# Kernel optimization log

Measured on AMD Instinct MI355X. Metric: run time of the kernel, lower is better.

## Reference

```python
import jax, jax.numpy as jnp
import numpy as np
import math

N_HEAD = 4
NORM_GROUPS = 32
EPS = 1e-5


def setup_inputs() -> dict:
    key = jax.random.key(0)
    ks = jax.random.split(key, 6)
    C = 256
    x = jax.random.normal(ks[0], (2, C, 64, 64), dtype=jnp.float32)
    gn_w = jnp.ones((C,), dtype=jnp.float32)
    gn_b = jnp.zeros((C,), dtype=jnp.float32)
    s = 1.0 / math.sqrt(C)
    wq = jax.random.normal(ks[1], (C, C), dtype=jnp.float32) * s
    wk = jax.random.normal(ks[2], (C, C), dtype=jnp.float32) * s
    wv = jax.random.normal(ks[3], (C, C), dtype=jnp.float32) * s
    wo = jax.random.normal(ks[4], (C, C), dtype=jnp.float32) * s
    bo = jnp.zeros((C,), dtype=jnp.float32)
    return {"x": x, "gn_w": gn_w, "gn_b": gn_b, "wq": wq, "wk": wk,
            "wv": wv, "wo": wo, "bo": bo}


def group_norm(x, w, b):
    bsz, c, h, wd = x.shape
    xg = x.reshape(bsz, NORM_GROUPS, c // NORM_GROUPS, h, wd)
    mu = jnp.mean(xg, axis=(2, 3, 4), keepdims=True)
    var = jnp.mean(jnp.square(xg - mu), axis=(2, 3, 4), keepdims=True)
    xn = ((xg - mu) * jax.lax.rsqrt(var + EPS)).reshape(bsz, c, h, wd)
    return xn * w[None, :, None, None] + b[None, :, None, None]


def conv1x1(x, w):
    # w: (out_ch, in_ch) applied pointwise
    return jnp.einsum('bchw,oc->bohw', x, w)


def reference(x, gn_w, gn_b, wq, wk, wv, wo, bo):
    bsz, c, h, w = x.shape
    hd = c // N_HEAD
    norm = group_norm(x, gn_w, gn_b)
    q = conv1x1(norm, wq).reshape(bsz, N_HEAD, hd, h, w)
    k = conv1x1(norm, wk).reshape(bsz, N_HEAD, hd, h, w)
    v = conv1x1(norm, wv).reshape(bsz, N_HEAD, hd, h, w)
    # scores over full spatial positions; NOTE: scaled by sqrt(channel), as in source
    scores = jnp.einsum('bnchw,bncxy->bnhwxy', q, k) / jnp.sqrt(jnp.float32(c))
    probs = jax.nn.softmax(scores.reshape(bsz, N_HEAD, h, w, h * w), axis=-1)
    probs = probs.reshape(bsz, N_HEAD, h, w, h, w)
    out = jnp.einsum('bnhwxy,bncxy->bnchw', probs, v).reshape(bsz, c, h, w)
    out = conv1x1(out, wo) + bo[None, :, None, None]
    return out + x
```

## Files before the change

### kernel.cpp

```cpp
#include <hip/hip_runtime.h>

typedef float f32x4 __attribute__((ext_vector_type(4)));
typedef float f32x16 __attribute__((ext_vector_type(16)));
typedef short bf16x8 __attribute__((ext_vector_type(8)));
typedef unsigned short u16;
typedef unsigned int u32;
typedef unsigned int u32x2 __attribute__((ext_vector_type(2)));

#define MFMA(a, b, c) __builtin_amdgcn_mfma_f32_16x16x32_bf16((a), (b), (c), 0, 0, 0)
#define MFMA32(a, b, c) __builtin_amdgcn_mfma_f32_32x32x16_bf16((a), (b), (c), 0, 0, 0)

static __device__ __forceinline__ u16 f2bf(float f) {
    union { float f; u32 u; } v; v.f = f;
    u32 r = v.u + 0x7FFFu + ((v.u >> 16) & 1u);
    return (u16)(r >> 16);
}

static __device__ __forceinline__ u32 pkbf(float a, float b) {
    u32 ua = __float_as_uint(a) + 0x8000u;
    u32 ub = __float_as_uint(b) + 0x8000u;
    return __builtin_amdgcn_perm(ub, ua, 0x07060302);
}

#define BAR_LGKM() do { \
    asm volatile("s_waitcnt lgkmcnt(0)" ::: "memory"); \
    __builtin_amdgcn_s_barrier(); \
} while (0)

__global__ __launch_bounds__(256) void prep_kernel(
    const float* __restrict__ wq, const float* __restrict__ wk,
    const float* __restrict__ wv, const float* __restrict__ wo,
    const float* __restrict__ x, u16* __restrict__ Wbf,
    float2* __restrict__ part) {
    int blk = blockIdx.x;
    int t = threadIdx.x;
    if (blk < 256) {
        int base = (blk * 256 + t) * 4;
        int p = base >> 16;
        int off = base & 65535;
        const float* W = (p == 0) ? wq : ((p == 1) ? wk : ((p == 2) ? wv : wo));
        float sc = (p == 0) ? 0.09014009048f : 1.0f;
        float4 v = *(const float4*)(W + off);
        uint2 pk;
        pk.x = pkbf(v.x * sc, v.y * sc);
        pk.y = pkbf(v.z * sc, v.w * sc);
        *(uint2*)(Wbf + base) = pk;
        return;
    }
    int sblk = blk - 256;
    int bg = sblk >> 2, quarter = sblk & 3;
    const float* xp = x + (size_t)bg * 32768 + quarter * 8192;

    float s = 0.f, ss = 0.f;
#pragma unroll
    for (int rep = 0; rep < 8; ++rep) {
        float4 v = *(const float4*)(xp + t * 4 + rep * 1024);
        s += v.x + v.y + v.z + v.w;
        ss += v.x * v.x + v.y * v.y + v.z * v.z + v.w * v.w;
    }
    for (int off = 1; off < 64; off <<= 1) {
        s += __shfl_xor(s, off);
        ss += __shfl_xor(ss, off);
    }
    __shared__ float red[8];
    int lane = t & 63, w = t >> 6;
    if (lane == 0) { red[w] = s; red[4 + w] = ss; }
    __syncthreads();
    if (t == 0) {
        part[sblk] = make_float2(red[0] + red[1] + red[2] + red[3],
                                 red[4] + red[5] + red[6] + red[7]);
    }
}

__global__ __launch_bounds__(256) void qkv_gemm(
    const float* __restrict__ x, const float* __restrict__ gw,
    const float* __restrict__ gb, const float2* __restrict__ part,
    const u16* __restrict__ Wbf,
    u16* __restrict__ Q, u16* __restrict__ K, u16* __restrict__ V) {
    int b = blockIdx.y & 1;
    int p = blockIdx.y >> 1;
    const u16* W = Wbf + p * 65536;
    int m0 = (blockIdx.x & 1) * 128;
    int n0 = (blockIdx.x >> 1) * 64;

    __shared__ u16 a_s[128 * 40];
    __shared__ u16 b_s[64 * 40];
    __shared__ float wgt_s[256], bia_s[256];

    int t = threadIdx.x;
    int lane = t & 63, wave = t >> 6;
    int wm = wave & 1, wn = wave >> 1;
    int r = lane & 15, qd = lane >> 4;

    {
        int c = t;
        int g = c >> 3;
        float s = 0.f, ss = 0.f;
#pragma unroll
        for (int q = 0; q < 4; ++q) {
            float2 pp = part[(b * 32 + g) * 4 + q];
            s += pp.x; ss += pp.y;
        }
        float mu = s * (1.f / 32768.f);
        float var = ss * (1.f / 32768.f) - mu * mu;
        float rstd = rsqrtf(var + 1e-5f);
        float wg = gw[c] * rstd;
        wgt_s[c] = wg;
        bia_s[c] = gb[c] - mu * wg;
    }
    __syncthreads();

    f32x4 acc[4][2];
#pragma unroll
    for (int i = 0; i < 4; ++i)
#pragma unroll
        for (int j = 0; j < 2; ++j) acc[i][j] = (f32x4){0.f, 0.f, 0.f, 0.f};

    int srow = t >> 1;
    int scp = (t & 1) * 16;
    int cb = t & 31;
    int s4 = (t >> 5) * 4;

    for (int kk = 0; kk < 256; kk += 32) {
        __syncthreads();
        {
            const u16* src = W + (m0 + srow) * 256 + kk + scp;
            *(uint4*)(a_s + srow * 40 + scp) = *(const uint4*)(src);
            *(uint4*)(a_s + srow * 40 + scp + 8) = *(const uint4*)(src + 8);
        }
        {
            int c = kk + cb;
            float wg = wgt_s[c], bi = bia_s[c];
            const float* xsrc = x + (size_t)(b * 256 + c) * 4096 + n0;
            float4 v0 = *(const float4*)(xsrc + s4);
            float4 v1 = *(const float4*)(xsrc + s4 + 32);
            u16* d0 = b_s + s4 * 40 + cb;
            d0[0]   = f2bf(v0.x * wg + bi);
            d0[40]  = f2bf(v0.y * wg + bi);
            d0[80]  = f2bf(v0.z * wg + bi);
            d0[120] = f2bf(v0.w * wg + bi);
            u16* d1 = b_s + (s4 + 32) * 40 + cb;
            d1[0]   = f2bf(v1.x * wg + bi);
            d1[40]  = f2bf(v1.y * wg + bi);
            d1[80]  = f2bf(v1.z * wg + bi);
            d1[120] = f2bf(v1.w * wg + bi);
        }
        __syncthreads();

        bf16x8 af[4], bf[2];
#pragma unroll
        for (int mt = 0; mt < 4; ++mt)
            af[mt] = *(const bf16x8*)(a_s + (wm * 64 + mt * 16 + r) * 40 + qd * 8);
#pragma unroll
        for (int nt = 0; nt < 2; ++nt)
            bf[nt] = *(const bf16x8*)(b_s + (wn * 32 + nt * 16 + r) * 40 + qd * 8);
        if (p == 2) {
#pragma unroll
            for (int mt = 0; mt < 4; ++mt)
#pragma unroll
                for (int nt = 0; nt < 2; ++nt)
                    acc[mt][nt] = MFMA(bf[nt], af[mt], acc[mt][nt]);
        } else {
#pragma unroll
            for (int mt = 0; mt < 4; ++mt)
#pragma unroll
                for (int nt = 0; nt < 2; ++nt)
                    acc[mt][nt] = MFMA(af[mt], bf[nt], acc[mt][nt]);
        }
    }

    if (p < 2) {
        u16* dst = (p == 0) ? Q : K;
#pragma unroll
        for (int mt = 0; mt < 4; ++mt) {
#pragma unroll
            for (int nt = 0; nt < 2; ++nt) {
                int o0 = m0 + wm * 64 + mt * 16 + qd * 4;
                int s = n0 + wn * 32 + nt * 16 + r;
                int h = o0 >> 6, d0 = o0 & 63;
                uint2 pk;
                pk.x = pkbf(acc[mt][nt][0], acc[mt][nt][1]);
                pk.y = pkbf(acc[mt][nt][2], acc[mt][nt][3]);
                *(uint2*)(dst + ((size_t)((b * 4 + h) * 4096 + s)) * 64 + d0) = pk;
            }
        }
    } else {
#pragma unroll
        for (int mt = 0; mt < 4; ++mt) {
#pragma unroll
            for (int nt = 0; nt < 2; ++nt) {
                int o = m0 + wm * 64 + mt * 16 + r;
                int h = o >> 6, d = o & 63;
                int sb = n0 + wn * 32 + nt * 16 + qd * 4;
                uint2 pk;
                pk.x = pkbf(acc[mt][nt][0], acc[mt][nt][1]);
                pk.y = pkbf(acc[mt][nt][2], acc[mt][nt][3]);
                *(uint2*)(V + ((size_t)((b * 4 + h) * 64 + d)) * 4096 + sb) = pk;
            }
        }
    }
}

template <int QT>
__global__ __launch_bounds__(256, 2) void attn_kernel(
    const u16* __restrict__ Q, const u16* __restrict__ K,
    const u16* __restrict__ V, u16* __restrict__ Opart,
    float* __restrict__ Lpart, int nk32) {
    int bh = blockIdx.x & 7, sp = blockIdx.x >> 3;
    int qb = blockIdx.y;
    int t = threadIdx.x, lane = t & 63, w = t >> 6;
    int qn = lane & 31, h = lane >> 5;

    const size_t bhoff = (size_t)bh * 4096 * 64;
    int q0 = (qb * 4 + w) * (32 * QT);
    int kbase = sp * nk32 * 32;

    __shared__ u16 smem[16384];

    bf16x8 qf[QT][4];
#pragma unroll
    for (int qt = 0; qt < QT; ++qt)
#pragma unroll
        for (int c = 0; c < 4; ++c)
            qf[qt][c] = *(const bf16x8*)(Q + bhoff +
                (size_t)(q0 + qt * 32 + qn) * 64 + c * 16 + h * 8);

    f32x16 oacc[2][QT];
#pragma unroll
    for (int dt = 0; dt < 2; ++dt)
#pragma unroll
        for (int qt = 0; qt < QT; ++qt)
#pragma unroll
            for (int i = 0; i < 16; ++i) oacc[dt][qt][i] = 0.f;
    float lacc[QT];
#pragma unroll
    for (int qt = 0; qt < QT; ++qt) lacc[qt] = 0.f;

    const u16* Kp = K + bhoff;
    const u16* Vp = V + bhoff;

    int srow = t >> 3, sg = t & 7;
    int ssw = (srow & 7);
    uint4 stg[4];

    auto load_pair = [&](int kp) {
        stg[0] = *(const uint4*)(Kp + (size_t)(kp + srow) * 64 + sg * 8);
        stg[1] = *(const uint4*)(Kp + (size_t)(kp + srow + 32) * 64 + sg * 8);
        stg[2] = *(const uint4*)(Vp + (size_t)srow * 4096 + kp + sg * 8);
        stg[3] = *(const uint4*)(Vp + (size_t)(srow + 32) * 4096 + kp + sg * 8);
    };
    auto write_pair = [&](u16* buf) {
        int gd = (sg ^ ssw) << 3;
        *(uint4*)(buf + srow * 64 + gd) = stg[0];
        *(uint4*)(buf + (srow + 32) * 64 + gd) = stg[1];
        *(uint4*)(buf + 4096 + srow * 64 + gd) = stg[2];
        *(uint4*)(buf + 4096 + (srow + 32) * 64 + gd) = stg[3];
    };

    int sw = qn & 7;
    auto step = [&](const u16* buf, int j) {
        bf16x8 kf[4], vf[2][2];
        int kr = j * 32 + qn;
#pragma unroll
        for (int c = 0; c < 4; ++c)
            kf[c] = *(const bf16x8*)(buf + kr * 64 + (((c * 2 + h) ^ sw) << 3));
#pragma unroll
        for (int dt = 0; dt < 2; ++dt) {
            int d = dt * 32 + qn;
#pragma unroll
            for (int kc = 0; kc < 2; ++kc) {
                int g = j * 4 + kc * 2 + h;
                vf[dt][kc] = *(const bf16x8*)(buf + 4096 + d * 64 + ((g ^ sw) << 3));
            }
        }
#pragma unroll
        for (int qt = 0; qt < QT; ++qt) {
            f32x16 s;
#pragma unroll
            for (int i = 0; i < 16; ++i) s[i] = 0.f;
            __builtin_amdgcn_s_setprio(1);
#pragma unroll
            for (int c = 0; c < 4; ++c) s = MFMA32(kf[c], qf[qt][c], s);
            __builtin_amdgcn_s_setprio(0);

            float e[16];
#pragma unroll
            for (int i = 0; i < 16; ++i)
                e[i] = __builtin_amdgcn_exp2f(s[i]);
            float t0 = (e[0] + e[1]) + (e[2] + e[3]);
            float t1 = (e[4] + e[5]) + (e[6] + e[7]);
            float t2 = (e[8] + e[9]) + (e[10] + e[11]);
            float t3 = (e[12] + e[13]) + (e[14] + e[15]);
            lacc[qt] += (t0 + t1) + (t2 + t3);

            u32 p[8];
#pragma unroll
            for (int i = 0; i < 8; ++i) p[i] = pkbf(e[2 * i], e[2 * i + 1]);

            u32x2 r0 = __builtin_amdgcn_permlane32_swap(p[0], p[2], false, false);
            u32x2 r1 = __builtin_amdgcn_permlane32_swap(p[1], p[3], false, false);
            u32x2 r2 = __builtin_amdgcn_permlane32_swap(p[4], p[6], false, false);
            u32x2 r3 = __builtin_amdgcn_permlane32_swap(p[5], p[7], false, false);
            uint4 pau = {r0[0], r1[0], r0[1], r1[1]};
            uint4 pbu = {r2[0], r3[0], r2[1], r3[1]};
            bf16x8 pA = *(const bf16x8*)&pau;
            bf16x8 pB = *(const bf16x8*)&pbu;

            __builtin_amdgcn_s_setprio(1);
#pragma unroll
            for (int dt = 0; dt < 2; ++dt) {
                oacc[dt][qt] = MFMA32(vf[dt][0], pA, oacc[dt][qt]);
                oacc[dt][qt] = MFMA32(vf[dt][1], pB, oacc[dt][qt]);
            }
            __builtin_amdgcn_s_setprio(0);
        }
    };

    int npair = nk32 >> 1;
    load_pair(kbase);
    write_pair(smem);
    if (npair > 1) load_pair(kbase + 64);
    BAR_LGKM();

    for (int i = 0; i < npair; ++i) {
        u16* cur = smem + (i & 1) * 8192;
        u16* nxt = smem + ((i + 1) & 1) * 8192;
        step(cur, 0);
        if (i + 1 < npair) write_pair(nxt);
        step(cur, 1);
        if (i + 2 < npair) load_pair(kbase + (i + 2) * 64);
        BAR_LGKM();
    }

    float lfull[QT];
#pragma unroll
    for (int qt = 0; qt < QT; ++qt)
        lfull[qt] = lacc[qt] + __shfl_xor(lacc[qt], 32);

    u16* my = smem + w * (32 * 72);
    size_t obase = ((size_t)sp * 8 + bh) * 4096 + q0;
#pragma unroll
    for (int qt = 0; qt < QT; ++qt) {
#pragma unroll
        for (int dt = 0; dt < 2; ++dt) {
#pragma unroll
            for (int g = 0; g < 4; ++g) {
                int d0 = g * 8 + h * 4 + dt * 32;
                uint2 pk;
                pk.x = pkbf(oacc[dt][qt][4 * g], oacc[dt][qt][4 * g + 1]);
                pk.y = pkbf(oacc[dt][qt][4 * g + 2], oacc[dt][qt][4 * g + 3]);
                *(uint2*)(my + qn * 72 + d0) = pk;
            }
        }
#pragma unroll
        for (int rr = 0; rr < 4; ++rr) {
            int row = rr * 8 + (lane >> 3), ch = lane & 7;
            uint4 v = *(const uint4*)(my + row * 72 + ch * 8);
            *(uint4*)(Opart + (obase + qt * 32 + row) * 64 + ch * 8) = v;
        }
    }
    if (h == 0) {
#pragma unroll
        for (int qt = 0; qt < QT; ++qt)
            Lpart[obase + qt * 32 + qn] = lfull[qt];
    }
}

__global__ __launch_bounds__(256) void attn_combine(
    const u16* __restrict__ Opart, const float* __restrict__ Lpart,
    u16* __restrict__ attnT, int nsplit) {
    int t = threadIdx.x;
    int gr = blockIdx.x * 64 + (t >> 2);
    int d0 = (t & 3) * 16;

    float l = 0.f;
    for (int s = 0; s < nsplit; ++s) l += Lpart[(size_t)s * 32768 + gr];
    float inv = 1.f / l;

    float acc[16];
#pragma unroll
    for (int i = 0; i < 16; ++i) acc[i] = 0.f;
    for (int s = 0; s < nsplit; ++s) {
        const u16* p = Opart + ((size_t)s * 32768 + gr) * 64 + d0;
        uint4 a = *(const uint4*)(p);
        uint4 bq = *(const uint4*)(p + 8);
        const u32* ap = (const u32*)&a;
        const u32* bp = (const u32*)&bq;
#pragma unroll
        for (int j = 0; j < 4; ++j) {
            acc[2 * j]     += __uint_as_float(ap[j] << 16);
            acc[2 * j + 1] += __uint_as_float(ap[j] & 0xFFFF0000u);
            acc[8 + 2 * j]     += __uint_as_float(bp[j] << 16);
            acc[8 + 2 * j + 1] += __uint_as_float(bp[j] & 0xFFFF0000u);
        }
    }
    u32 pk[8];
#pragma unroll
    for (int j = 0; j < 8; ++j)
        pk[j] = pkbf(acc[2 * j] * inv, acc[2 * j + 1] * inv);

    int bh = gr >> 12, q = gr & 4095;
    int b = bh >> 2, hh = bh & 3;
    u16* dst = attnT + ((size_t)(b * 4096 + q)) * 256 + hh * 64 + d0;
    *(uint4*)(dst) = make_uint4(pk[0], pk[1], pk[2], pk[3]);
    *(uint4*)(dst + 8) = make_uint4(pk[4], pk[5], pk[6], pk[7]);
}

__global__ __launch_bounds__(256) void out_gemm(
    const u16* __restrict__ attnT, const u16* __restrict__ W3,
    const float* __restrict__ bo, const float* __restrict__ x,
    float* __restrict__ out) {
    int b = blockIdx.y;
    int m0 = (blockIdx.x & 3) * 64;
    int n0 = (blockIdx.x >> 2) * 64;

    __shared__ u16 a_s[64 * 40];
    __shared__ u16 b_s[64 * 40];

    int t = threadIdx.x;
    int lane = t & 63, wave = t >> 6;
    int wm = wave & 1, wn = wave >> 1;
    int r = lane & 15, qd = lane >> 4;

    const u16* Bsrc = attnT + (size_t)b * 4096 * 256;

    f32x4 acc[2][2];
#pragma unroll
    for (int i = 0; i < 2; ++i)
#pragma unroll
        for (int j = 0; j < 2; ++j) acc[i][j] = (f32x4){0.f, 0.f, 0.f, 0.f};

    int u = t & 127;
    int srow = u >> 1;
    int scp = (u & 1) * 16;

    for (int kk = 0; kk < 256; kk += 32) {
        __syncthreads();
        if (t < 128) {
            const u16* src = W3 + (m0 + srow) * 256 + kk + scp;
            *(uint4*)(a_s + srow * 40 + scp) = *(const uint4*)(src);
            *(uint4*)(a_s + srow * 40 + scp + 8) = *(const uint4*)(src + 8);
        } else {
            const u16* src = Bsrc + (size_t)(n0 + srow) * 256 + kk + scp;
            *(uint4*)(b_s + srow * 40 + scp) = *(const uint4*)(src);
            *(uint4*)(b_s + srow * 40 + scp + 8) = *(const uint4*)(src + 8);
        }
        __syncthreads();

        bf16x8 af[2], bf[2];
#pragma unroll
        for (int mt = 0; mt < 2; ++mt)
            af[mt] = *(const bf16x8*)(a_s + (wm * 32 + mt * 16 + r) * 40 + qd * 8);
#pragma unroll
        for (int nt = 0; nt < 2; ++nt)
            bf[nt] = *(const bf16x8*)(b_s + (wn * 32 + nt * 16 + r) * 40 + qd * 8);
#pragma unroll
        for (int mt = 0; mt < 2; ++mt)
#pragma unroll
            for (int nt = 0; nt < 2; ++nt)
                acc[mt][nt] = MFMA(af[mt], bf[nt], acc[mt][nt]);
    }

#pragma unroll
    for (int mt = 0; mt < 2; ++mt) {
#pragma unroll
        for (int nt = 0; nt < 2; ++nt) {
#pragma unroll
            for (int j = 0; j < 4; ++j) {
                int o = m0 + wm * 32 + mt * 16 + qd * 4 + j;
                int s = n0 + wn * 32 + nt * 16 + r;
                size_t idx = (size_t)(b * 256 + o) * 4096 + s;
                out[idx] = acc[mt][nt][j] + bo[o] + x[idx];
            }
        }
    }
}

extern "C" void kernel_launch(void* const* d_in, const int* in_sizes, int n_in,
                              void* d_out, int out_size, void* d_ws, size_t ws_size,
                              hipStream_t stream) {
    const float* x = (const float*)d_in[0];
    const float* gn_w = (const float*)d_in[1];
    const float* gn_b = (const float*)d_in[2];
    const float* wq = (const float*)d_in[3];
    const float* wk = (const float*)d_in[4];
    const float* wv = (const float*)d_in[5];
    const float* wo = (const float*)d_in[6];
    const float* bo = (const float*)d_in[7];
    float* out = (float*)d_out;

    char* ws = (char*)d_ws;
    u16* attnT = (u16*)(ws);
    u16* Q     = (u16*)(ws + (4u << 20));
    u16* Kp    = (u16*)(ws + (8u << 20));
    u16* Vp    = (u16*)(ws + (12u << 20));
    u16* Wbf   = (u16*)(ws + (16u << 20));
    float2* part = (float2*)(ws + (16u << 20) + 524288);

    size_t opart_off = (size_t)17 << 20;
    size_t osplit = 8ull * 4096 * 64 * 2;
    int nsplit;
    if (ws_size >= opart_off + 8 * osplit + 8ull * 32768 * 4 + 4096) nsplit = 8;
    else if (ws_size >= opart_off + 4 * osplit + 4ull * 32768 * 4 + 4096) nsplit = 4;
    else nsplit = 2;
    u16* Opart = (u16*)(ws + opart_off);
    float* Lpart = (float*)(ws + opart_off + (size_t)nsplit * osplit);

    prep_kernel<<<512, 256, 0, stream>>>(wq, wk, wv, wo, x, Wbf, part);
    qkv_gemm<<<dim3(128, 6), 256, 0, stream>>>(x, gn_w, gn_b, part, Wbf, Q, Kp, Vp);
    attn_kernel<2><<<dim3(8 * nsplit, 16), 256, 0, stream>>>(
        Q, Kp, Vp, Opart, Lpart, 128 / nsplit);
    attn_combine<<<512, 256, 0, stream>>>(Opart, Lpart, attnT, nsplit);
    out_gemm<<<dim3(256, 2), 256, 0, stream>>>(attnT, Wbf + 3 * 65536, bo, x, out);
}
```

Before: 161.2 us.

## Stream K/V tiles straight into LDS with global_load_lds double buffering

The attention kernel used to stage K/V tiles through registers and then write them to LDS. It now issues direct global-to-LDS loads (global_load_lds, 16 bytes per lane), with each wave filling one quarter of a tile and the XOR swizzle applied on the global source address. The pipeline is restructured so that after each barrier the freed buffer is refilled two steps ahead, and the barrier waits on vmcnt instead of lgkmcnt. This frees the staging VGPRs and removes the ds_write instructions, but each barrier now waits for all outstanding global loads, which could expose memory latency.

```diff
diff --git a/kernel.cpp b/kernel.cpp
--- a/kernel.cpp
+++ b/kernel.cpp
@@ -22,9 +22,16 @@
     return __builtin_amdgcn_perm(ub, ua, 0x07060302);
 }
 
-#define BAR_LGKM() do { \
-    asm volatile("s_waitcnt lgkmcnt(0)" ::: "memory"); \
+static __device__ __forceinline__ void gll16(const u16* g, u16* l) {
+    __builtin_amdgcn_global_load_lds(
+        (const __attribute__((address_space(1))) u32*)(const void*)g,
+        (__attribute__((address_space(3))) u32*)(void*)l, 16, 0, 0);
+}
+
+#define BAR_VM() do { \
+    asm volatile("s_waitcnt vmcnt(0)" ::: "memory"); \
     __builtin_amdgcn_s_barrier(); \
+    asm volatile("" ::: "memory"); \
 } while (0)
 
 __global__ __launch_bounds__(256) void prep_kernel(
@@ -239,22 +246,20 @@
     const u16* Kp = K + bhoff;
     const u16* Vp = V + bhoff;
 
-    int srow = t >> 3, sg = t & 7;
-    int ssw = (srow & 7);
-    uint4 stg[4];
-
-    auto load_pair = [&](int kp) {
-        stg[0] = *(const uint4*)(Kp + (size_t)(kp + srow) * 64 + sg * 8);
-        stg[1] = *(const uint4*)(Kp + (size_t)(kp + srow + 32) * 64 + sg * 8);
-        stg[2] = *(const uint4*)(Vp + (size_t)srow * 4096 + kp + sg * 8);
-        stg[3] = *(const uint4*)(Vp + (size_t)(srow + 32) * 4096 + kp + sg * 8);
-    };
-    auto write_pair = [&](u16* buf) {
-        int gd = (sg ^ ssw) << 3;
-        *(uint4*)(buf + srow * 64 + gd) = stg[0];
-        *(uint4*)(buf + (srow + 32) * 64 + gd) = stg[1];
-        *(uint4*)(buf + 4096 + srow * 64 + gd) = stg[2];
-        *(uint4*)(buf + 4096 + (srow + 32) * 64 + gd) = stg[3];
+    int gs = (lane & 7) ^ (lane >> 3);
+    int rbase = (w & 1) * 32 + (lane >> 3);
+
+    auto fill = [&](int bufsel, int kp) {
+        u16* ld = smem + bufsel * 8192 + w * 2048;
+        if (w < 2) {
+            const u16* s = Kp + (size_t)(kp + rbase) * 64 + gs * 8;
+#pragma unroll
+            for (int j = 0; j < 4; ++j) gll16(s + j * 512, ld + j * 512);
+        } else {
+            const u16* s = Vp + (size_t)rbase * 4096 + kp + gs * 8;
+#pragma unroll
+            for (int j = 0; j < 4; ++j) gll16(s + j * 32768, ld + j * 512);
+        }
     };
 
     int sw = qn & 7;
@@ -317,19 +322,16 @@
     };
 
     int npair = nk32 >> 1;
-    load_pair(kbase);
-    write_pair(smem);
-    if (npair > 1) load_pair(kbase + 64);
-    BAR_LGKM();
+    fill(0, kbase);
+    if (npair > 1) fill(1, kbase + 64);
+    BAR_VM();
 
     for (int i = 0; i < npair; ++i) {
-        u16* cur = smem + (i & 1) * 8192;
-        u16* nxt = smem + ((i + 1) & 1) * 8192;
+        const u16* cur = smem + (i & 1) * 8192;
         step(cur, 0);
-        if (i + 1 < npair) write_pair(nxt);
         step(cur, 1);
-        if (i + 2 < npair) load_pair(kbase + (i + 2) * 64);
-        BAR_LGKM();
+        BAR_VM();
+        if (i + 2 < npair) fill(i & 1, kbase + (i + 2) * 64);
     }
 
     float lfull[QT];
```

After: 145.1 us. 10.0% less time.
